# Kernel tuning notes

Measured on AMD Instinct MI355X. Metric: run time of the kernel, lower is better.

The kernel has to match this reference:

```python
import jax, jax.numpy as jnp
import numpy as np

BN_EPS = 1e-5
K2 = 9  # 3x3 kernel


def _conv3x3(x, w, b):
    # x: [B,C,H,W], w: [O,C,3,3] -> [B,O,H,W], stride 1, pad 1
    out = jax.lax.conv_general_dilated(
        x, w, window_strides=(1, 1), padding=((1, 1), (1, 1)),
        dimension_numbers=("NCHW", "OIHW", "NCHW"))
    return out + b[None, :, None, None]


def setup_inputs() -> dict:
    key = jax.random.key(0)
    ks = jax.random.split(key, 8)
    B, C, H, W = 8, 256, 64, 64
    O = 256
    x = jax.random.normal(ks[0], (B, C, H, W), dtype=jnp.float32)
    # offset/mask conv: small init so sampled offsets stay near the base grid
    w_off = jax.random.normal(ks[1], (3 * K2, C, 3, 3), dtype=jnp.float32) * 0.01
    b_off = jnp.zeros((3 * K2,), dtype=jnp.float32)
    weight = jax.random.normal(ks[2], (O, C, 3, 3), dtype=jnp.float32) * 0.02
    bias = jnp.zeros((O,), dtype=jnp.float32)
    gamma = jnp.ones((O,), dtype=jnp.float32)
    beta = jnp.zeros((O,), dtype=jnp.float32)
    run_mean = jax.random.normal(ks[3], (O,), dtype=jnp.float32) * 0.1
    run_var = jax.random.uniform(ks[4], (O,), dtype=jnp.float32) + 0.5
    return {"x": x, "w_off": w_off, "b_off": b_off, "weight": weight,
            "bias": bias, "gamma": gamma, "beta": beta,
            "run_mean": run_mean, "run_var": run_var}


def _deform_sample(img, py, px):
    # img: [C,H,W]; py, px: [K2,H,W] sampling coordinates.
    # Bilinear sample with zero padding outside (DCNv2 semantics:
    # out-of-bounds corners contribute zero).
    C, H, W = img.shape
    y0 = jnp.floor(py)
    x0 = jnp.floor(px)
    wy1 = py - y0  # frac weights for the 'high' corner
    wx1 = px - x0

    def gather(yi, xi):
        valid = (yi >= 0) & (yi < H) & (xi >= 0) & (xi < W)
        yc = jnp.clip(yi, 0, H - 1).astype(jnp.int32)
        xc = jnp.clip(xi, 0, W - 1).astype(jnp.int32)
        return img[:, yc, xc] * valid.astype(img.dtype)[None]  # [C,K2,H,W]

    v00 = gather(y0, x0)
    v01 = gather(y0, x0 + 1)
    v10 = gather(y0 + 1, x0)
    v11 = gather(y0 + 1, x0 + 1)
    return (v00 * ((1 - wy1) * (1 - wx1))[None]
            + v01 * ((1 - wy1) * wx1)[None]
            + v10 * (wy1 * (1 - wx1))[None]
            + v11 * (wy1 * wx1)[None])  # [C,K2,H,W]


def reference(x, w_off, b_off, weight, bias, gamma, beta, run_mean, run_var):
    B, C, H, W = x.shape
    O = weight.shape[0]
    # 1) offset / mask branch (standard 3x3 conv)
    om = _conv3x3(x, w_off, b_off)  # [B, 27, H, W]
    off_y = om[:, :K2]
    off_x = om[:, K2:2 * K2]
    mask = jax.nn.sigmoid(om[:, 2 * K2:])  # modulation, [B,9,H,W]
    # 2) base sampling grid for 3x3, stride 1, pad 1, dilation 1
    ky = jnp.repeat(jnp.arange(3), 3).astype(x.dtype)  # [9]
    kx = jnp.tile(jnp.arange(3), 3).astype(x.dtype)    # [9]
    hs = jnp.arange(H, dtype=x.dtype)
    ws = jnp.arange(W, dtype=x.dtype)
    base_y = hs[None, :, None] - 1.0 + ky[:, None, None]  # [9,H,1]
    base_x = ws[None, None, :] - 1.0 + kx[:, None, None]  # [9,1,W]
    py = base_y[None] + off_y  # [B,9,H,W]
    px = base_x[None] + off_x
    # 3) modulated deformable im2col (bilinear gather) per batch
    cols = jax.vmap(_deform_sample)(x, py, px)  # [B,C,9,H,W]
    cols = cols * mask[:, None]                 # apply modulation mask
    # 4) GEMM over (C, K2) + bias
    w3 = weight.reshape(O, C, K2)
    out = jnp.einsum("ock,bckhw->bohw", w3, cols) + bias[None, :, None, None]
    # 5) BatchNorm (eval mode, running stats) + ReLU
    inv = gamma / jnp.sqrt(run_var + BN_EPS)
    out = out * inv[None, :, None, None] + (beta - run_mean * inv)[None, :, None, None]
    return jax.nn.relu(out)
```

## Files before the change

kernel.cpp:

```cpp
#include <hip/hip_runtime.h>
#include <math.h>

#define H 64
#define W 64
#define C 256
#define O 256
#define CK 2304
#define NB 8
#define HWSZ 4096

typedef __attribute__((ext_vector_type(8))) short short8;
typedef __attribute__((ext_vector_type(4))) float floatx4;

#define FSWZ(n) ((((n) & 3) << 1) | (((n) >> 2) & 1))

__device__ __forceinline__ unsigned short f2bf(float f) {
  unsigned u = __builtin_bit_cast(unsigned, f);
  unsigned r = (u + 0x7fffu + ((u >> 16) & 1u)) >> 16;
  return (unsigned short)r;
}
__device__ __forceinline__ float bf2f(short s) {
  unsigned u = ((unsigned)(unsigned short)s) << 16;
  return __builtin_bit_cast(float, u);
}

__global__ __launch_bounds__(256) void transpose_x(
    const float* __restrict__ x, unsigned short* __restrict__ xt) {
  __shared__ unsigned tile[64 * 65];
  int b = blockIdx.x, y = blockIdx.y, cg = blockIdx.z;
  int tid = threadIdx.x;
  const float* xb = x + ((size_t)b * C + cg * 128) * HWSZ + y * W;
#pragma unroll 4
  for (int it = 0; it < 16; ++it) {
    int e = tid + 256 * it;
    int xx = e & 63;
    int cp = e >> 6;
    float f0 = xb[(size_t)(2 * cp) * HWSZ + xx];
    float f1 = xb[(size_t)(2 * cp + 1) * HWSZ + xx];
    tile[cp * 65 + xx] = (unsigned)f2bf(f0) | ((unsigned)f2bf(f1) << 16);
  }
  __syncthreads();
  unsigned short* xo = xt + ((size_t)(b * 64 + y) << 14) + cg * 128;
#pragma unroll
  for (int it = 0; it < 4; ++it) {
    int e = tid + 256 * it;
    int cq = e & 15;
    int xx = e >> 4;
    unsigned u0 = tile[(cq * 4 + 0) * 65 + xx];
    unsigned u1 = tile[(cq * 4 + 1) * 65 + xx];
    unsigned u2 = tile[(cq * 4 + 2) * 65 + xx];
    unsigned u3 = tile[(cq * 4 + 3) * 65 + xx];
    uint4 v = {u0, u1, u2, u3};
    *reinterpret_cast<uint4*>(xo + (xx << 8) + (cq << 3)) = v;
  }
}

__global__ __launch_bounds__(256) void prep_weight(
    const float* __restrict__ weight, unsigned short* __restrict__ wb) {
  int d0 = (blockIdx.x * 256 + threadIdx.x) * 2;
  unsigned short v[2];
#pragma unroll
  for (int e = 0; e < 2; ++e) {
    int d = d0 + e;
    int j = d & 7;
    int lane = (d >> 3) & 63;
    int mt = (d >> 9) & 15;
    int ks = d >> 13;
    int o = mt * 16 + (lane & 15);
    int kn = ks * 32 + (lane >> 4) * 8 + j;
    int tap = kn >> 8;
    int c = kn & 255;
    v[e] = f2bf(weight[o * CK + c * 9 + tap]);
  }
  *reinterpret_cast<unsigned*>(wb + d0) =
      (unsigned)v[0] | ((unsigned)v[1] << 16);
}

__global__ __launch_bounds__(256) void prep_woff(
    const float* __restrict__ w_off, unsigned short* __restrict__ wob) {
  int d0 = (blockIdx.x * 256 + threadIdx.x) * 2;
  unsigned short v[2];
#pragma unroll
  for (int e = 0; e < 2; ++e) {
    int d = d0 + e;
    int j = d & 7;
    int lane = (d >> 3) & 63;
    int mt = (d >> 9) & 1;
    int ks = d >> 10;
    int o = mt * 16 + (lane & 15);
    int kn = ks * 32 + (lane >> 4) * 8 + j;
    int tap = kn >> 8;
    int c = kn & 255;
    v[e] = (o < 27) ? f2bf(w_off[o * CK + c * 9 + tap]) : (unsigned short)0;
  }
  *reinterpret_cast<unsigned*>(wob + d0) =
      (unsigned)v[0] | ((unsigned)v[1] << 16);
}

__global__ __launch_bounds__(256) void prep_bn(
    const float* __restrict__ bias, const float* __restrict__ gamma,
    const float* __restrict__ beta, const float* __restrict__ run_mean,
    const float* __restrict__ run_var, float* __restrict__ invsh) {
  int o = threadIdx.x;
  float inv = gamma[o] * rsqrtf(run_var[o] + 1e-5f);
  invsh[o] = inv;
  invsh[O + o] = beta[o] + (bias[o] - run_mean[o]) * inv;
}

__global__ __launch_bounds__(256, 4) void offset_mfma_kernel(
    const unsigned short* __restrict__ xt, const unsigned short* __restrict__ wob,
    const float* __restrict__ b_off, float* __restrict__ om) {
  int tid = threadIdx.x;
  int lane = tid & 63;
  int wvid = tid >> 6;
  int nt = wvid & 1;
  int mt = wvid >> 1;
  int q = lane >> 4;
  int lm = lane & 15;
  int b = blockIdx.x;
  int h = blockIdx.y;
  int half = blockIdx.z;
  const unsigned short* xtb = xt + ((size_t)b << 20);

  floatx4 acc = (floatx4){0.f, 0.f, 0.f, 0.f};
  int px = half * 32 + nt * 16 + lm;

  for (int tap = 0; tap < 9; ++tap) {
    int yy = h - 1 + tap / 3;
    int xx = px - 1 + tap % 3;
    bool v = (yy >= 0) && (yy < H) && (xx >= 0) && (xx < W);
    const unsigned short* bp =
        xtb + ((((yy & 63) << 6) + (xx & 63)) << 8) + q * 8;
#pragma unroll
    for (int s = 0; s < 8; ++s) {
      int ks = tap * 8 + s;
      short8 bfrag;
      if (v)
        bfrag = *reinterpret_cast<const short8*>(bp + s * 32);
      else
        bfrag = (short8){0, 0, 0, 0, 0, 0, 0, 0};
      short8 afrag = *reinterpret_cast<const short8*>(
          wob + (((ks * 2 + mt) * 64 + lane) << 3));
      acc = __builtin_amdgcn_mfma_f32_16x16x32_bf16(afrag, bfrag, acc, 0, 0, 0);
    }
  }
#pragma unroll
  for (int r = 0; r < 4; ++r) {
    int o = mt * 16 + q * 4 + r;
    if (o < 27)
      om[((b * 27 + o) * H + h) * W + px] = acc[r] + b_off[o];
  }
}

__global__ __launch_bounds__(512, 4) void deform_mfma_kernel(
    const unsigned short* __restrict__ xt, const float* __restrict__ om,
    const unsigned short* __restrict__ wb, const float* __restrict__ invsh,
    float* __restrict__ out) {
  __shared__ short cols[64 * 256];
  __shared__ int sbase[576];
  __shared__ float s00[576], s01[576], s10[576], s11[576];

  int tid = threadIdx.x;
  int lane = tid & 63;
  int wvid = tid >> 6;
  int mg = wvid >> 1;
  int nh = wvid & 1;
  int q = lane >> 4;
  int lm = lane & 15;
  int b = blockIdx.x;
  int h = blockIdx.y;
  const unsigned short* xtb = xt + ((size_t)b << 20);

  for (int e = tid; e < 576; e += 512) {
    int n = e & 63;
    int k = e >> 6;
    int base = ((b * 27 + k) * H + h) * W + n;
    float oy = om[base];
    float ox = om[base + 9 * HWSZ];
    float mv = om[base + 18 * HWSZ];
    float m = 1.0f / (1.0f + __expf(-mv));
    float py = (float)(h - 1 + k / 3) + oy;
    float px = (float)(n - 1 + k % 3) + ox;
    float yf = floorf(py), xf = floorf(px);
    int y0 = (int)yf, x0 = (int)xf;
    float fy = py - yf, fx = px - xf;
    float r0, r1; int yl;
    if (y0 >= 0 && y0 <= H - 2)      { yl = y0;    r0 = 1.f - fy; r1 = fy;       }
    else if (y0 == -1)               { yl = 0;     r0 = fy;       r1 = 0.f;      }
    else if (y0 == H - 1)            { yl = H - 2; r0 = 0.f;      r1 = 1.f - fy; }
    else                             { yl = 0;     r0 = 0.f;      r1 = 0.f;      }
    float c0, c1; int xl;
    if (x0 >= 0 && x0 <= W - 2)      { xl = x0;    c0 = 1.f - fx; c1 = fx;       }
    else if (x0 == -1)               { xl = 0;     c0 = fx;       c1 = 0.f;      }
    else if (x0 == W - 1)            { xl = W - 2; c0 = 0.f;      c1 = 1.f - fx; }
    else                             { xl = 0;     c0 = 0.f;      c1 = 0.f;      }
    r0 *= m; r1 *= m;
    sbase[e] = ((yl << 6) + xl) << 8;
    s00[e] = r0 * c0; s01[e] = r0 * c1;
    s10[e] = r1 * c0; s11[e] = r1 * c1;
  }
  __syncthreads();

  floatx4 acc[4][2];
#pragma unroll
  for (int a = 0; a < 4; ++a)
#pragma unroll
    for (int u = 0; u < 2; ++u) acc[a][u] = (floatx4){0.f, 0.f, 0.f, 0.f};

  int sn = tid >> 3;
  int scb = tid & 7;

  for (int tap = 0; tap < 9; ++tap) {
    if (tap) __syncthreads();
    {
      int ei = tap * 64 + sn;
      int base = sbase[ei];
      float w00 = s00[ei], w01 = s01[ei], w10 = s10[ei], w11 = s11[ei];
      const unsigned short* p = xtb + base;
#pragma unroll
      for (int i = 0; i < 4; ++i) {
        int cbw = (i << 3) | scb;
        int co = cbw << 3;
        short8 f00 = *reinterpret_cast<const short8*>(p + co);
        short8 f01 = *reinterpret_cast<const short8*>(p + 256 + co);
        short8 f10 = *reinterpret_cast<const short8*>(p + 16384 + co);
        short8 f11 = *reinterpret_cast<const short8*>(p + 16640 + co);
        short8 pk;
#pragma unroll
        for (int j = 0; j < 8; ++j) {
          float v = w00 * bf2f(f00[j]) + w01 * bf2f(f01[j]) +
                    w10 * bf2f(f10[j]) + w11 * bf2f(f11[j]);
          pk[j] = (short)f2bf(v);
        }
        int pos = (cbw ^ FSWZ(sn)) & 31;
        *reinterpret_cast<short8*>(&cols[(sn << 8) + (pos << 3)]) = pk;
      }
    }
    __syncthreads();

#pragma unroll
    for (int s = 0; s < 8; ++s) {
      int ks = tap * 8 + s;
      short8 afrag[4];
#pragma unroll
      for (int a = 0; a < 4; ++a)
        afrag[a] = *reinterpret_cast<const short8*>(
            wb + (((ks * 16 + mg * 4 + a) * 64 + lane) << 3));
      short8 bfrag[2];
#pragma unroll
      for (int u = 0; u < 2; ++u) {
        int nn = (nh * 2 + u) * 16 + lm;
        int pos = ((s * 4 + q) ^ FSWZ(nn)) & 31;
        bfrag[u] = *reinterpret_cast<const short8*>(&cols[(nn << 8) + (pos << 3)]);
      }
#pragma unroll
      for (int a = 0; a < 4; ++a)
#pragma unroll
        for (int u = 0; u < 2; ++u)
          acc[a][u] = __builtin_amdgcn_mfma_f32_16x16x32_bf16(
              afrag[a], bfrag[u], acc[a][u], 0, 0, 0);
    }
  }

#pragma unroll
  for (int a = 0; a < 4; ++a) {
#pragma unroll
    for (int u = 0; u < 2; ++u) {
      int nn = (nh * 2 + u) * 16 + lm;
#pragma unroll
      for (int r = 0; r < 4; ++r) {
        int o = (mg * 4 + a) * 16 + q * 4 + r;
        float v = fmaf(acc[a][u][r], invsh[o], invsh[O + o]);
        out[((size_t)(b * O + o)) * HWSZ + h * W + nn] = fmaxf(v, 0.0f);
      }
    }
  }
}

extern "C" void kernel_launch(void* const* d_in, const int* in_sizes, int n_in,
                              void* d_out, int out_size, void* d_ws, size_t ws_size,
                              hipStream_t stream) {
  const float* x        = (const float*)d_in[0];
  const float* w_off    = (const float*)d_in[1];
  const float* b_off    = (const float*)d_in[2];
  const float* weight   = (const float*)d_in[3];
  const float* bias     = (const float*)d_in[4];
  const float* gamma    = (const float*)d_in[5];
  const float* beta     = (const float*)d_in[6];
  const float* run_mean = (const float*)d_in[7];
  const float* run_var  = (const float*)d_in[8];
  float* out = (float*)d_out;

  char* ws = (char*)d_ws;
  unsigned short* xt = (unsigned short*)ws;
  float* om  = (float*)(ws + 16777216);
  unsigned short* wbf = (unsigned short*)(ws + 20316160);
  unsigned short* wob = (unsigned short*)(ws + 21495808);
  float* invsh = (float*)(ws + 21643264);

  {
    dim3 grid(NB, H, 2);
    transpose_x<<<grid, 256, 0, stream>>>(x, xt);
  }
  prep_weight<<<O * CK / 512, 256, 0, stream>>>(weight, wbf);
  prep_woff<<<32 * CK / 512, 256, 0, stream>>>(w_off, wob);
  prep_bn<<<1, 256, 0, stream>>>(bias, gamma, beta, run_mean, run_var, invsh);

  {
    dim3 grid(NB, H, 2);
    offset_mfma_kernel<<<grid, 256, 0, stream>>>(xt, wob, b_off, om);
  }
  {
    dim3 grid(NB, H);
    deform_mfma_kernel<<<grid, 512, 0, stream>>>(xt, om, wbf, invsh, out);
  }
}
```

Measured before the change: 212.5 us.

## Fuse offset conv into deformable kernel and pack bilinear interpolation on bf16 pairs

The offset/mask convolution now runs inside the deformable kernel. Each block computes its row's 27x64 offsets with MFMA into shared memory, which removes one launch and the global round trip of the om buffer. The bilinear sampling loop now reads the bf16 values as packed uint pairs, uses explicit fmaf, and rounds back to bf16 with a simpler round-half-up on pairs. This cuts conversion instructions but changes rounding from round-to-nearest-even, and it adds shared memory and offset work to each deform block.

Result: no change. 208.7 us (-1.8%).

```diff
diff --git a/kernel.cpp b/kernel.cpp
--- a/kernel.cpp
+++ b/kernel.cpp
@@ -11,6 +11,7 @@
 
 typedef __attribute__((ext_vector_type(8))) short short8;
 typedef __attribute__((ext_vector_type(4))) float floatx4;
+typedef __attribute__((ext_vector_type(4))) unsigned uintx4;
 
 #define FSWZ(n) ((((n) & 3) << 1) | (((n) >> 2) & 1))
 
@@ -19,9 +20,16 @@
   unsigned r = (u + 0x7fffu + ((u >> 16) & 1u)) >> 16;
   return (unsigned short)r;
 }
-__device__ __forceinline__ float bf2f(short s) {
-  unsigned u = ((unsigned)(unsigned short)s) << 16;
-  return __builtin_bit_cast(float, u);
+__device__ __forceinline__ float lo2f(unsigned u) {
+  return __builtin_bit_cast(float, u << 16);
+}
+__device__ __forceinline__ float hi2f(unsigned u) {
+  return __builtin_bit_cast(float, u & 0xffff0000u);
+}
+__device__ __forceinline__ unsigned pk2bf(float v0, float v1) {
+  unsigned a = __builtin_bit_cast(unsigned, v0);
+  unsigned b = __builtin_bit_cast(unsigned, v1);
+  return ((a + 0x8000u) >> 16) | ((b + 0x8000u) & 0xffff0000u);
 }
 
 __global__ __launch_bounds__(256) void transpose_x(
@@ -107,77 +115,62 @@
   invsh[O + o] = beta[o] + (bias[o] - run_mean[o]) * inv;
 }
 
-__global__ __launch_bounds__(256, 4) void offset_mfma_kernel(
+__global__ __launch_bounds__(512, 4) void deform_mfma_kernel(
     const unsigned short* __restrict__ xt, const unsigned short* __restrict__ wob,
-    const float* __restrict__ b_off, float* __restrict__ om) {
+    const float* __restrict__ b_off, const unsigned short* __restrict__ wb,
+    const float* __restrict__ invsh, float* __restrict__ out) {
+  __shared__ short cols[64 * 256];
+  __shared__ float sm_om[27 * 64];
+  __shared__ int sbase[576];
+  __shared__ float s00[576], s01[576], s10[576], s11[576];
+
   int tid = threadIdx.x;
   int lane = tid & 63;
   int wvid = tid >> 6;
-  int nt = wvid & 1;
-  int mt = wvid >> 1;
-  int q = lane >> 4;
-  int lm = lane & 15;
-  int b = blockIdx.x;
-  int h = blockIdx.y;
-  int half = blockIdx.z;
-  const unsigned short* xtb = xt + ((size_t)b << 20);
-
-  floatx4 acc = (floatx4){0.f, 0.f, 0.f, 0.f};
-  int px = half * 32 + nt * 16 + lm;
-
-  for (int tap = 0; tap < 9; ++tap) {
-    int yy = h - 1 + tap / 3;
-    int xx = px - 1 + tap % 3;
-    bool v = (yy >= 0) && (yy < H) && (xx >= 0) && (xx < W);
-    const unsigned short* bp =
-        xtb + ((((yy & 63) << 6) + (xx & 63)) << 8) + q * 8;
-#pragma unroll
-    for (int s = 0; s < 8; ++s) {
-      int ks = tap * 8 + s;
-      short8 bfrag;
-      if (v)
-        bfrag = *reinterpret_cast<const short8*>(bp + s * 32);
-      else
-        bfrag = (short8){0, 0, 0, 0, 0, 0, 0, 0};
-      short8 afrag = *reinterpret_cast<const short8*>(
-          wob + (((ks * 2 + mt) * 64 + lane) << 3));
-      acc = __builtin_amdgcn_mfma_f32_16x16x32_bf16(afrag, bfrag, acc, 0, 0, 0);
-    }
-  }
-#pragma unroll
-  for (int r = 0; r < 4; ++r) {
-    int o = mt * 16 + q * 4 + r;
-    if (o < 27)
-      om[((b * 27 + o) * H + h) * W + px] = acc[r] + b_off[o];
-  }
-}
-
-__global__ __launch_bounds__(512, 4) void deform_mfma_kernel(
-    const unsigned short* __restrict__ xt, const float* __restrict__ om,
-    const unsigned short* __restrict__ wb, const float* __restrict__ invsh,
-    float* __restrict__ out) {
-  __shared__ short cols[64 * 256];
-  __shared__ int sbase[576];
-  __shared__ float s00[576], s01[576], s10[576], s11[576];
-
-  int tid = threadIdx.x;
-  int lane = tid & 63;
-  int wvid = tid >> 6;
-  int mg = wvid >> 1;
-  int nh = wvid & 1;
   int q = lane >> 4;
   int lm = lane & 15;
   int b = blockIdx.x;
   int h = blockIdx.y;
   const unsigned short* xtb = xt + ((size_t)b << 20);
 
+  {
+    int mt = wvid & 1;
+    int nt = wvid >> 1;
+    floatx4 acc0 = (floatx4){0.f, 0.f, 0.f, 0.f};
+    int px = nt * 16 + lm;
+    for (int tap = 0; tap < 9; ++tap) {
+      int yy = h - 1 + tap / 3;
+      int xx = px - 1 + tap % 3;
+      bool v = (yy >= 0) && (yy < H) && (xx >= 0) && (xx < W);
+      const unsigned short* bp =
+          xtb + ((((yy & 63) << 6) + (xx & 63)) << 8) + q * 8;
+#pragma unroll
+      for (int s = 0; s < 8; ++s) {
+        int ks = tap * 8 + s;
+        short8 bfrag;
+        if (v)
+          bfrag = *reinterpret_cast<const short8*>(bp + s * 32);
+        else
+          bfrag = (short8){0, 0, 0, 0, 0, 0, 0, 0};
+        short8 afrag = *reinterpret_cast<const short8*>(
+            wob + (((ks * 2 + mt) * 64 + lane) << 3));
+        acc0 = __builtin_amdgcn_mfma_f32_16x16x32_bf16(afrag, bfrag, acc0, 0, 0, 0);
+      }
+    }
+#pragma unroll
+    for (int r = 0; r < 4; ++r) {
+      int o = mt * 16 + q * 4 + r;
+      if (o < 27) sm_om[o * 64 + px] = acc0[r] + b_off[o];
+    }
+  }
+  __syncthreads();
+
   for (int e = tid; e < 576; e += 512) {
     int n = e & 63;
     int k = e >> 6;
-    int base = ((b * 27 + k) * H + h) * W + n;
-    float oy = om[base];
-    float ox = om[base + 9 * HWSZ];
-    float mv = om[base + 18 * HWSZ];
+    float oy = sm_om[k * 64 + n];
+    float ox = sm_om[(9 + k) * 64 + n];
+    float mv = sm_om[(18 + k) * 64 + n];
     float m = 1.0f / (1.0f + __expf(-mv));
     float py = (float)(h - 1 + k / 3) + oy;
     float px = (float)(n - 1 + k % 3) + ox;
@@ -202,6 +195,8 @@
   __syncthreads();
 
   floatx4 acc[4][2];
+  int mg = wvid >> 1;
+  int nh = wvid & 1;
 #pragma unroll
   for (int a = 0; a < 4; ++a)
 #pragma unroll
@@ -221,19 +216,23 @@
       for (int i = 0; i < 4; ++i) {
         int cbw = (i << 3) | scb;
         int co = cbw << 3;
-        short8 f00 = *reinterpret_cast<const short8*>(p + co);
-        short8 f01 = *reinterpret_cast<const short8*>(p + 256 + co);
-        short8 f10 = *reinterpret_cast<const short8*>(p + 16384 + co);
-        short8 f11 = *reinterpret_cast<const short8*>(p + 16640 + co);
-        short8 pk;
-#pragma unroll
-        for (int j = 0; j < 8; ++j) {
-          float v = w00 * bf2f(f00[j]) + w01 * bf2f(f01[j]) +
-                    w10 * bf2f(f10[j]) + w11 * bf2f(f11[j]);
-          pk[j] = (short)f2bf(v);
+        uintx4 u00 = *reinterpret_cast<const uintx4*>(p + co);
+        uintx4 u01 = *reinterpret_cast<const uintx4*>(p + 256 + co);
+        uintx4 u10 = *reinterpret_cast<const uintx4*>(p + 16384 + co);
+        uintx4 u11 = *reinterpret_cast<const uintx4*>(p + 16640 + co);
+        uintx4 res;
+#pragma unroll
+        for (int jd = 0; jd < 4; ++jd) {
+          float v0 = fmaf(w00, lo2f(u00[jd]),
+                     fmaf(w01, lo2f(u01[jd]),
+                     fmaf(w10, lo2f(u10[jd]), w11 * lo2f(u11[jd]))));
+          float v1 = fmaf(w00, hi2f(u00[jd]),
+                     fmaf(w01, hi2f(u01[jd]),
+                     fmaf(w10, hi2f(u10[jd]), w11 * hi2f(u11[jd]))));
+          res[jd] = pk2bf(v0, v1);
         }
         int pos = (cbw ^ FSWZ(sn)) & 31;
-        *reinterpret_cast<short8*>(&cols[(sn << 8) + (pos << 3)]) = pk;
+        *reinterpret_cast<uintx4*>(&cols[(sn << 8) + (pos << 3)]) = res;
       }
     }
     __syncthreads();
@@ -293,10 +292,9 @@
 
   char* ws = (char*)d_ws;
   unsigned short* xt = (unsigned short*)ws;
-  float* om  = (float*)(ws + 16777216);
-  unsigned short* wbf = (unsigned short*)(ws + 20316160);
-  unsigned short* wob = (unsigned short*)(ws + 21495808);
-  float* invsh = (float*)(ws + 21643264);
+  unsigned short* wbf = (unsigned short*)(ws + 16777216);
+  unsigned short* wob = (unsigned short*)(ws + 17956864);
+  float* invsh = (float*)(ws + 18104320);
 
   {
     dim3 grid(NB, H, 2);
@@ -307,11 +305,7 @@
   prep_bn<<<1, 256, 0, stream>>>(bias, gamma, beta, run_mean, run_var, invsh);
 
   {
-    dim3 grid(NB, H, 2);
-    offset_mfma_kernel<<<grid, 256, 0, stream>>>(xt, wob, b_off, om);
-  }
-  {
     dim3 grid(NB, H);
-    deform_mfma_kernel<<<grid, 512, 0, stream>>>(xt, om, wbf, invsh, out);
-  }
-}
+    deform_mfma_kernel<<<grid, 512, 0, stream>>>(xt, wob, b_off, wbf, invsh, out);
+  }
+}
```
